# Performance work log

Measured on AMD Instinct MI355X. Metric: run time of the kernel, lower is better.

The kernel has to match this reference:

```python
import math
import jax, jax.numpy as jnp
import numpy as np

HEAD_DIM = 128
NUM_HEADS = 16
NUM_KV_HEADS = 4
CAUSAL = True


def rotate_half(x):
    x1 = x[..., : x.shape[-1] // 2]
    x2 = x[..., x.shape[-1] // 2 :]
    return jnp.concatenate([-x2, x1], axis=-1)


def setup_inputs() -> dict:
    key = jax.random.key(0)
    k1, k2, k3, k4, k5 = jax.random.split(key, 5)
    B, S, H = 2, 2048, 2048
    total_heads = NUM_HEADS + 2 * NUM_KV_HEADS  # 24
    hidden_states = jax.random.normal(k1, (B, S, H), dtype=jnp.float32)
    cos = jax.random.normal(k2, (S, HEAD_DIM), dtype=jnp.float32)
    sin = jax.random.normal(k3, (S, HEAD_DIM), dtype=jnp.float32)
    # eqx.nn.Linear weight layout: [out_features, in_features], y = W @ x
    w_qkv = jax.random.normal(k4, (total_heads * HEAD_DIM, H), dtype=jnp.float32) / math.sqrt(H)
    w_o = jax.random.normal(k5, (H, NUM_HEADS * HEAD_DIM), dtype=jnp.float32) / math.sqrt(NUM_HEADS * HEAD_DIM)
    return {"hidden_states": hidden_states, "cos": cos, "sin": sin, "w_qkv": w_qkv, "w_o": w_o}


def reference(hidden_states, cos, sin, w_qkv, w_o):
    B, S, _ = hidden_states.shape
    # fused QKV projection: [B,S,total_heads,head_dim]
    qkv = jnp.einsum("bsh,oh->bso", hidden_states, w_qkv).reshape(B, S, -1, HEAD_DIM)
    q = qkv[:, :, :NUM_HEADS]
    k = qkv[:, :, NUM_HEADS : NUM_HEADS + NUM_KV_HEADS]
    v = qkv[:, :, NUM_HEADS + NUM_KV_HEADS :]
    # RoPE: cos/sin [S,head_dim] -> broadcast [S,1,head_dim] over heads
    c = cos[..., None, :]
    s_ = sin[..., None, :]
    q = q * c + rotate_half(q) * s_
    k = k * c + rotate_half(k) * s_
    # GQA: repeat K/V across query-head groups
    rep = NUM_HEADS // NUM_KV_HEADS
    k = jnp.repeat(k, rep, axis=2)
    v = jnp.repeat(v, rep, axis=2)
    scale = 1.0 / math.sqrt(HEAD_DIM)
    scores = jnp.einsum("bshd,bthd->bhst", q, k) * scale  # [B,H,S,S]
    if CAUSAL:
        mask = jnp.tril(jnp.ones((S, S), dtype=bool))[None, None]
        scores = jnp.where(mask, scores, jnp.float32(-1e10))
    attn = jax.nn.softmax(scores, axis=-1)
    out = jnp.einsum("bhst,bthd->bshd", attn, v).reshape(B, S, -1)
    return jnp.einsum("bsd,od->bso", out, w_o)
```

## Files before the change

kernel.cpp:

```cpp
#include <hip/hip_runtime.h>
#include <hip/hip_bf16.h>
#include <stdint.h>

typedef __hip_bfloat16 bf16;
typedef __attribute__((ext_vector_type(8))) __bf16 bf16x8;
typedef __attribute__((ext_vector_type(4))) float f32x4;
typedef __attribute__((ext_vector_type(16))) float f32x16;
typedef __attribute__((ext_vector_type(4))) unsigned int u32x4;

#define QSCALE_LOG2E (0.08838834764831845f * 1.4426950408889634f)

__device__ __forceinline__ float fast_exp2(float x) {
#if __has_builtin(__builtin_amdgcn_exp2f)
  return __builtin_amdgcn_exp2f(x);
#else
  return exp2f(x);
#endif
}

__device__ __forceinline__ void gload_lds16(const void* g, void* l) {
  __builtin_amdgcn_global_load_lds(
      (__attribute__((address_space(1))) void*)(uintptr_t)g,
      (__attribute__((address_space(3))) void*)(uint32_t)(uintptr_t)l,
      16, 0, 0);
}

__global__ void cast3(const float* __restrict__ h, const float* __restrict__ wq,
                      const float* __restrict__ wo, bf16* __restrict__ oh,
                      bf16* __restrict__ owq, bf16* __restrict__ owo) {
  const int total = 4718592;
  const int stride = gridDim.x * blockDim.x;
  for (int c = blockIdx.x * blockDim.x + threadIdx.x; c < total; c += stride) {
    const float* src;
    bf16* dst;
    int i;
    if (c < 2097152) { src = h; dst = oh; i = c; }
    else if (c < 3670016) { src = wq; dst = owq; i = c - 2097152; }
    else { src = wo; dst = owo; i = c - 3670016; }
    float4 v = reinterpret_cast<const float4*>(src)[i];
    bf16 tmp[4];
    tmp[0] = __float2bfloat16(v.x);
    tmp[1] = __float2bfloat16(v.y);
    tmp[2] = __float2bfloat16(v.z);
    tmp[3] = __float2bfloat16(v.w);
    reinterpret_cast<uint2*>(dst)[i] = *reinterpret_cast<uint2*>(tmp);
  }
}

__device__ __forceinline__ void store_c(float v, bf16* p) { *p = __float2bfloat16(v); }
__device__ __forceinline__ void store_c(float v, float* p) { *p = v; }

__device__ __forceinline__ bf16x8 rd_swz(const bf16* base, int row, int ks, int hi) {
  const int byte = row * 128 + ((ks * 64 + hi * 16) ^ ((row & 7) << 4));
  return *reinterpret_cast<const bf16x8*>((const char*)base + byte);
}

__device__ __forceinline__ void stage_part(const bf16* __restrict__ g, int K,
                                           int kt, bf16* ldsBase, int part,
                                           int tid) {
  const int ga = part * 512 + tid;
  const int r = ga >> 3;
  const int gl = ga & 7;
  const int col = kt * 64 + ((gl ^ (r & 7)) << 3);
  gload_lds16(g + (size_t)r * K + col, (char*)ldsBase + ga * 16);
}

#define DS_A(QR)                                                              \
  _Pragma("unroll") for (int m = 0; m < 4; ++m)                               \
  _Pragma("unroll") for (int ks = 0; ks < 2; ++ks)                            \
      af[m][ks] = rd_swz(Acur, wm * 128 + (QR) * 64 + m * 16 + lr, ks, hi);

#define DS_B0()                                                               \
  _Pragma("unroll") for (int n = 0; n < NQ0; ++n)                             \
  _Pragma("unroll") for (int ks = 0; ks < 2; ++ks)                            \
      bf0[n][ks] = rd_swz(Bcur, wn * WN + n * 16 + lr, ks, hi);

#define DS_B1()                                                               \
  _Pragma("unroll") for (int n = 0; n < NQ1; ++n)                             \
  _Pragma("unroll") for (int ks = 0; ks < 2; ++ks)                            \
      bf1[n][ks] = rd_swz(Bcur, wn * WN + (NQ0 + n) * 16 + lr, ks, hi);

#define MFMA_Q0(QR)                                                           \
  __builtin_amdgcn_s_setprio(1);                                             \
  _Pragma("unroll") for (int ks = 0; ks < 2; ++ks)                            \
  _Pragma("unroll") for (int m = 0; m < 4; ++m)                               \
  _Pragma("unroll") for (int n = 0; n < NQ0; ++n)                             \
      acc[(QR) * 4 + m][n] = __builtin_amdgcn_mfma_f32_16x16x32_bf16(         \
          af[m][ks], bf0[n][ks], acc[(QR) * 4 + m][n], 0, 0, 0);              \
  __builtin_amdgcn_s_setprio(0);

#define MFMA_Q1(QR)                                                           \
  __builtin_amdgcn_s_setprio(1);                                             \
  _Pragma("unroll") for (int ks = 0; ks < 2; ++ks)                            \
  _Pragma("unroll") for (int m = 0; m < 4; ++m)                               \
  _Pragma("unroll") for (int n = 0; n < NQ1; ++n)                             \
      acc[(QR) * 4 + m][NQ0 + n] = __builtin_amdgcn_mfma_f32_16x16x32_bf16(   \
          af[m][ks], bf1[n][ks], acc[(QR) * 4 + m][NQ0 + n], 0, 0, 0);        \
  __builtin_amdgcn_s_setprio(0);

#define PHASE_SYNC_PRE()                                \
  __builtin_amdgcn_s_barrier();                         \
  asm volatile("s_waitcnt lgkmcnt(0)" ::: "memory");    \
  __builtin_amdgcn_sched_barrier(0);

#define PHASE_END() __builtin_amdgcn_s_barrier();

#define VMCNT_LB()                                                            \
  if constexpr (LB == 2) asm volatile("s_waitcnt vmcnt(2)" ::: "memory");     \
  else if constexpr (LB == 3) asm volatile("s_waitcnt vmcnt(3)" ::: "memory");\
  else asm volatile("s_waitcnt vmcnt(4)" ::: "memory");

template <int BN, typename OutT>
__global__ __launch_bounds__(512, 2) void gemm256(const bf16* __restrict__ A,
                                                  const bf16* __restrict__ B,
                                                  OutT* __restrict__ C,
                                                  int M, int N, int K, int NBX) {
  constexpr int NFRAG = BN / 64;
  constexpr int NQ0 = (NFRAG + 1) / 2;
  constexpr int NQ1 = NFRAG - NQ0;
  constexpr int WN = BN / 4;
  constexpr int LB = BN / 64;
  constexpr int LB0 = (LB + 1) / 2;
  constexpr int LB1 = LB - LB0;

  extern __shared__ bf16 sm[];
  bf16* A0 = sm;
  bf16* A1 = sm + 16384;
  bf16* B0 = sm + 32768;
  bf16* B1 = B0 + BN * 64;

  const int tid = threadIdx.x;
  const int lane = tid & 63;
  const int w = tid >> 6;
  const int wm = w >> 2;
  const int wn = w & 3;
  const int lr = lane & 15;
  const int hi = lane >> 4;

  const int nwg = gridDim.x;
  const int cpx = nwg >> 3;
  const int bid = blockIdx.x;
  const int wg = (bid & 7) * cpx + (bid >> 3);
  const int bx = wg % NBX;
  const int by = wg / NBX;
  const int row0 = by * 256;
  const int col0 = bx * BN;

  const bf16* Ag = A + (size_t)row0 * K;
  const bf16* Bg = B + (size_t)col0 * K;

#pragma unroll
  for (int p = 0; p < 4; ++p) stage_part(Ag, K, 0, A0, p, tid);
#pragma unroll
  for (int p = 0; p < LB; ++p) stage_part(Bg, K, 0, B0, p, tid);
#pragma unroll
  for (int p = 0; p < LB; ++p) stage_part(Bg, K, 1, B1, p, tid);
  VMCNT_LB();
  __builtin_amdgcn_s_barrier();

  f32x4 acc[8][NFRAG] = {};
  bf16x8 af[4][2], bf0[NQ0][2], bf1[NQ1 ? NQ1 : 1][2];

  const int iters = K >> 7;
  for (int i = 0; i < iters; ++i) {
    const bool g2 = (i + 1 < iters);
    const int t1 = 2 * i + 1, t2 = 2 * i + 2, t3 = 2 * i + 3;
    {
      const bf16* Acur = A0;
      const bf16* Bcur = B0;
      DS_A(0); DS_B0();
      stage_part(Ag, K, t1, A1, 0, tid);
      stage_part(Ag, K, t1, A1, 1, tid);
      PHASE_SYNC_PRE(); MFMA_Q0(0); PHASE_END();
      DS_B1();
      stage_part(Ag, K, t1, A1, 2, tid);
      stage_part(Ag, K, t1, A1, 3, tid);
      PHASE_SYNC_PRE(); MFMA_Q1(0); PHASE_END();
      DS_A(1);
      if (g2) {
#pragma unroll
        for (int p = 0; p < LB0; ++p) stage_part(Bg, K, t2, B0, p, tid);
      }
      PHASE_SYNC_PRE(); MFMA_Q0(1); PHASE_END();
      if (g2) {
#pragma unroll
        for (int p = 0; p < LB1; ++p) stage_part(Bg, K, t2, B0, LB0 + p, tid);
        VMCNT_LB();
      } else {
        asm volatile("s_waitcnt vmcnt(0)" ::: "memory");
      }
      PHASE_SYNC_PRE(); MFMA_Q1(1); PHASE_END();
    }
    {
      const bf16* Acur = A1;
      const bf16* Bcur = B1;
      DS_A(0); DS_B0();
      if (g2) {
        stage_part(Ag, K, t2, A0, 0, tid);
        stage_part(Ag, K, t2, A0, 1, tid);
      }
      PHASE_SYNC_PRE(); MFMA_Q0(0); PHASE_END();
      DS_B1();
      if (g2) {
        stage_part(Ag, K, t2, A0, 2, tid);
        stage_part(Ag, K, t2, A0, 3, tid);
      }
      PHASE_SYNC_PRE(); MFMA_Q1(0); PHASE_END();
      DS_A(1);
      if (g2) {
#pragma unroll
        for (int p = 0; p < LB0; ++p) stage_part(Bg, K, t3, B1, p, tid);
      }
      PHASE_SYNC_PRE(); MFMA_Q0(1); PHASE_END();
      if (g2) {
#pragma unroll
        for (int p = 0; p < LB1; ++p) stage_part(Bg, K, t3, B1, LB0 + p, tid);
        VMCNT_LB();
      } else {
        asm volatile("s_waitcnt vmcnt(0)" ::: "memory");
      }
      PHASE_SYNC_PRE(); MFMA_Q1(1); PHASE_END();
    }
  }

#pragma unroll
  for (int mi = 0; mi < 8; ++mi)
#pragma unroll
    for (int ni = 0; ni < NFRAG; ++ni)
#pragma unroll
      for (int j = 0; j < 4; ++j) {
        const int r = row0 + wm * 128 + mi * 16 + hi * 4 + j;
        const int cc = col0 + wn * WN + ni * 16 + lr;
        store_c(acc[mi][ni][j], &C[(size_t)r * N + cc]);
      }
}

__global__ __launch_bounds__(256) void rope_vtrans(const bf16* __restrict__ qkv,
                                                   const float* __restrict__ cs,
                                                   const float* __restrict__ sn,
                                                   bf16* __restrict__ Q,
                                                   bf16* __restrict__ Kd,
                                                   bf16* __restrict__ Vt) {
  __shared__ bf16 tile[64 * 136];
  const int bid = blockIdx.x;
  if (bid < 4096) {
    const int tok = bid;
    const int b = tok >> 11;
    const int s = tok & 2047;
    const bf16* row = qkv + (size_t)tok * 3072;
    for (int idx = threadIdx.x; idx < 1280; idx += blockDim.x) {
      const int head = idx >> 6;
      const int j = idx & 63;
      float x1 = __bfloat162float(row[head * 128 + j]);
      float x2 = __bfloat162float(row[head * 128 + j + 64]);
      const float c1 = cs[s * 128 + j];
      const float c2 = cs[s * 128 + j + 64];
      const float s1 = sn[s * 128 + j];
      const float s2 = sn[s * 128 + j + 64];
      float y1 = x1 * c1 - x2 * s1;
      float y2 = x2 * c2 + x1 * s2;
      bf16* dst;
      if (head < 16) {
        y1 *= QSCALE_LOG2E;
        y2 *= QSCALE_LOG2E;
        dst = Q + ((size_t)(b * 16 + head) * 2048 + s) * 128;
      } else {
        dst = Kd + ((size_t)(b * 4 + head - 16) * 2048 + s) * 128;
      }
      dst[j] = __float2bfloat16(y1);
      dst[j + 64] = __float2bfloat16(y2);
    }
  } else {
    const int vb = bid - 4096;
    const int stile = vb & 31;
    const int hv = (vb >> 5) & 3;
    const int b = vb >> 7;
    const int tid = threadIdx.x;
    const int tok0 = stile * 64;
    const bf16* src = qkv + (size_t)(b * 2048 + tok0) * 3072 + 2560 + hv * 128;
#pragma unroll
    for (int i = 0; i < 4; ++i) {
      const int c = tid + i * 256;
      const int r = c >> 4;
      const int off = (c & 15) * 8;
      uint4 d = *reinterpret_cast<const uint4*>(src + (size_t)r * 3072 + off);
      *reinterpret_cast<uint4*>(&tile[r * 136 + off]) = d;
    }
    __syncthreads();
    bf16* dst = Vt + ((size_t)(b * 4 + hv) * 128) * 2048 + tok0;
#pragma unroll
    for (int i = 0; i < 4; ++i) {
      const int o = tid + i * 256;
      const int d = o >> 3;
      const int s0 = (o & 7) * 8;
      bf16 vals[8];
#pragma unroll
      for (int j = 0; j < 8; ++j) vals[j] = tile[(s0 + j) * 136 + d];
      *reinterpret_cast<uint4*>(dst + (size_t)d * 2048 + s0) =
          *reinterpret_cast<const uint4*>(vals);
    }
  }
}

__device__ __forceinline__ void stage_k(const bf16* __restrict__ Kb, int k0,
                                        bf16* dst, int w, int lane) {
#pragma unroll
  for (int i = 0; i < 4; ++i) {
    const int L16 = i * 256 + w * 64 + lane;
    const int row = L16 >> 4;
    const int colb = (L16 & 15) * 16;
    const int src = colb ^ ((row & 7) << 4);
    gload_lds16(Kb + (size_t)(k0 + row) * 128 + (src >> 1),
                (char*)dst + (i * 256 + w * 64) * 16);
  }
}

__device__ __forceinline__ void stage_v(const bf16* __restrict__ Vtb, int k0,
                                        bf16* dst, int w, int lane) {
#pragma unroll
  for (int i = 0; i < 4; ++i) {
    const int L16 = i * 256 + w * 64 + lane;
    const int row = L16 >> 3;
    const int colb = (L16 & 7) * 16;
    const int src = colb ^ ((row & 7) << 4);
    gload_lds16(Vtb + (size_t)row * 2048 + k0 + (src >> 1),
                (char*)dst + (i * 256 + w * 64) * 16);
  }
}

__device__ __forceinline__ bf16x8 lds_read_swz(const bf16* base, int row,
                                               int colElem, int rowBytes) {
  const int byte = row * rowBytes + (((colElem * 2) ^ ((row & 7) << 4)));
  return *reinterpret_cast<const bf16x8*>((const char*)base + byte);
}

__global__ __launch_bounds__(256, 2) void attn_fwd(const bf16* __restrict__ Qg,
                                                   const bf16* __restrict__ Kg,
                                                   const bf16* __restrict__ Vtg,
                                                   bf16* __restrict__ Og) {
  __shared__ bf16 Ks[2][64 * 128];
  __shared__ bf16 Vs[2][128 * 64];

  const int tid = threadIdx.x;
  const int lane = tid & 63;
  const int w = tid >> 6;
  const int bid = blockIdx.x;
  int qt, bh;
  if (bid < 256) { qt = bid & 15; bh = bid >> 4; }
  else           { qt = 15 - (bid & 15); bh = 16 + ((bid - 256) >> 4); }
  const int b = bh >> 4;
  const int h = bh & 15;
  const int kvh = h >> 2;
  const int q31 = lane & 31;
  const int hw = lane >> 5;

  const bf16* Qb = Qg + ((size_t)(b * 16 + h) * 2048) * 128;
  const bf16* Kb = Kg + ((size_t)(b * 4 + kvh) * 2048) * 128;
  const bf16* Vtb = Vtg + ((size_t)(b * 4 + kvh) * 128) * 2048;

  const int qw = qt * 128 + w * 32;

  bf16x8 qf[8];
#pragma unroll
  for (int db = 0; db < 8; ++db)
    qf[db] = *reinterpret_cast<const bf16x8*>(Qb + (size_t)(qw + q31) * 128 +
                                              db * 16 + hw * 8);

  f32x16 acc[4] = {};
  float mrow = -1e30f;
  float lsum = 0.f;

  const int nt = 2 * qt + 2;

  stage_k(Kb, 0, &Ks[0][0], w, lane);
  stage_v(Vtb, 0, &Vs[0][0], w, lane);

  for (int t = 0; t < nt; ++t) {
    const int cur = t & 1;
    if (t + 1 < nt) {
      stage_k(Kb, (t + 1) * 64, &Ks[cur ^ 1][0], w, lane);
      stage_v(Vtb, (t + 1) * 64, &Vs[cur ^ 1][0], w, lane);
      asm volatile("s_waitcnt vmcnt(8)" ::: "memory");
    } else {
      asm volatile("s_waitcnt vmcnt(0)" ::: "memory");
    }
    __builtin_amdgcn_s_barrier();
    __builtin_amdgcn_sched_barrier(0);

    const int k0 = t * 64;
    const bool active = (k0 <= qw + 31);
    if (active) {
      const bf16* Kt = &Ks[cur][0];
      const bf16* Vtl = &Vs[cur][0];

      f32x16 sacc[2] = {};
#pragma unroll
      for (int kb = 0; kb < 2; ++kb)
#pragma unroll
        for (int db = 0; db < 8; ++db) {
          bf16x8 kf = lds_read_swz(Kt, kb * 32 + q31, db * 16 + hw * 8, 256);
          sacc[kb] = __builtin_amdgcn_mfma_f32_32x32x16_bf16(kf, qf[db],
                                                             sacc[kb], 0, 0, 0);
        }

      float p[2][16];
#pragma unroll
      for (int kb = 0; kb < 2; ++kb)
#pragma unroll
        for (int r = 0; r < 16; ++r) p[kb][r] = sacc[kb][r];

      if (k0 + 63 > qw) {
        const int qg = qw + q31;
#pragma unroll
        for (int kb = 0; kb < 2; ++kb)
#pragma unroll
          for (int r = 0; r < 16; ++r) {
            const int k = k0 + kb * 32 + (r & 3) + 8 * (r >> 2) + 4 * hw;
            if (k > qg) p[kb][r] = -1e30f;
          }
      }

      float mt = p[0][0];
#pragma unroll
      for (int r = 1; r < 16; ++r) mt = fmaxf(mt, p[0][r]);
#pragma unroll
      for (int r = 0; r < 16; ++r) mt = fmaxf(mt, p[1][r]);
      mt = fmaxf(mt, __shfl_xor(mt, 32));

      if (__any(mt > mrow + 11.5f)) {
        const float mnew = fmaxf(mrow, mt);
        const float alpha = fast_exp2(mrow - mnew);
        mrow = mnew;
        lsum *= alpha;
        float areg[16];
#pragma unroll
        for (int r = 0; r < 16; ++r) {
          const int qloc = (r & 3) + 8 * (r >> 2) + 4 * hw;
          areg[r] = __shfl(alpha, qloc + (lane & 32));
        }
#pragma unroll
        for (int db = 0; db < 4; ++db)
#pragma unroll
          for (int r = 0; r < 16; ++r) acc[db][r] *= areg[r];
      }

      float rs = 0.f;
#pragma unroll
      for (int kb = 0; kb < 2; ++kb)
#pragma unroll
        for (int r = 0; r < 16; ++r) {
          const float pe = fast_exp2(p[kb][r] - mrow);
          p[kb][r] = pe;
          rs += pe;
        }
      rs += __shfl_xor(rs, 32);
      lsum += rs;

      unsigned int pk[2][8];
#pragma unroll
      for (int kb = 0; kb < 2; ++kb)
#pragma unroll
        for (int i = 0; i < 8; ++i)
          asm("v_cvt_pk_bf16_f32 %0, %1, %2"
              : "=v"(pk[kb][i])
              : "v"(p[kb][2 * i]), "v"(p[kb][2 * i + 1]));

#pragma unroll
      for (int kb16 = 0; kb16 < 4; ++kb16) {
        const int kb = kb16 >> 1;
        const int j0 = (kb16 & 1) * 4;
        unsigned int a0 = pk[kb][j0 + 0], b0 = pk[kb][j0 + 2];
        unsigned int a1 = pk[kb][j0 + 1], b1 = pk[kb][j0 + 3];
        asm volatile("v_permlane32_swap_b32 %0, %1" : "+v"(a0), "+v"(b0));
        asm volatile("v_permlane32_swap_b32 %0, %1" : "+v"(a1), "+v"(b1));
        u32x4 afu;
        afu.x = a0; afu.y = a1; afu.z = b0; afu.w = b1;
        bf16x8 pa;
        __builtin_memcpy(&pa, &afu, 16);
#pragma unroll
        for (int db = 0; db < 4; ++db) {
          bf16x8 vf = lds_read_swz(Vtl, db * 32 + q31, kb16 * 16 + hw * 8, 128);
          acc[db] = __builtin_amdgcn_mfma_f32_32x32x16_bf16(pa, vf,
                                                            acc[db], 0, 0, 0);
        }
      }
    }

    __builtin_amdgcn_sched_barrier(0);
    __builtin_amdgcn_s_barrier();
  }

  const float inv = 1.0f / lsum;
  float invq[16];
#pragma unroll
  for (int r = 0; r < 16; ++r) {
    const int qloc = (r & 3) + 8 * (r >> 2) + 4 * hw;
    invq[r] = __shfl(inv, qloc + (lane & 32));
  }
#pragma unroll
  for (int db = 0; db < 4; ++db)
#pragma unroll
    for (int r = 0; r < 16; ++r) {
      const int qg = qw + (r & 3) + 8 * (r >> 2) + 4 * hw;
      const int dg = db * 32 + q31;
      Og[((size_t)(b * 2048 + qg)) * 2048 + h * 128 + dg] =
          __float2bfloat16(acc[db][r] * invq[r]);
    }
}

extern "C" void kernel_launch(void* const* d_in, const int* in_sizes, int n_in,
                              void* d_out, int out_size, void* d_ws,
                              size_t ws_size, hipStream_t stream) {
  const float* hidden = (const float*)d_in[0];
  const float* cs = (const float*)d_in[1];
  const float* sn = (const float*)d_in[2];
  const float* wqkv = (const float*)d_in[3];
  const float* wo = (const float*)d_in[4];
  float* out = (float*)d_out;

  bf16* p = (bf16*)d_ws;
  bf16* hid_b = p;   p += 8388608;
  bf16* wqkv_b = p;  p += 6291456;
  bf16* wo_b = p;    p += 4194304;
  bf16* qkv = p;     p += 12582912;
  bf16* Qs = p;      p += 8388608;
  bf16* Ksc = p;     p += 2097152;
  bf16* Vt = p;      p += 2097152;

  (void)hipFuncSetAttribute((const void*)gemm256<192, bf16>,
                            hipFuncAttributeMaxDynamicSharedMemorySize, 131072);
  (void)hipFuncSetAttribute((const void*)gemm256<128, float>,
                            hipFuncAttributeMaxDynamicSharedMemorySize, 131072);

  cast3<<<2048, 256, 0, stream>>>(hidden, wqkv, wo, hid_b, wqkv_b, wo_b);

  gemm256<192, bf16><<<256, 512, 114688, stream>>>(hid_b, wqkv_b, qkv,
                                                   4096, 3072, 2048, 16);
  rope_vtrans<<<4352, 256, 0, stream>>>(qkv, cs, sn, Qs, Ksc, Vt);

  bf16* aout = hid_b;
  attn_fwd<<<512, 256, 0, stream>>>(Qs, Ksc, Vt, aout);

  gemm256<128, float><<<256, 512, 98304, stream>>>(aout, wo_b, out,
                                                   4096, 2048, 2048, 16);
}
```

Measured before the change: 173.1 us.

## Store transposed V in 8-token chunked layout for contiguous LDS staging

The V transpose kernel now writes V in a blocked layout: for each group of 8 tokens, every head-dim row holds a contiguous 16-byte chunk. The attention kernel stages V tiles with fully contiguous 16-byte global-to-LDS loads and reads LDS fragments without the XOR swizzle. This is meant to improve global coalescing for V loads, since the old layout used strided 2048-element rows, and to drop the swizzle arithmetic. LDS reads are now unswizzled, which could raise bank conflicts.

Result: no change. 171.5 us (-0.9%).

```diff
diff --git a/kernel.cpp b/kernel.cpp
--- a/kernel.cpp
+++ b/kernel.cpp
@@ -287,16 +287,17 @@
       *reinterpret_cast<uint4*>(&tile[r * 136 + off]) = d;
     }
     __syncthreads();
-    bf16* dst = Vt + ((size_t)(b * 4 + hv) * 128) * 2048 + tok0;
+    bf16* dst8 = Vt + ((size_t)(b * 4 + hv) * 128) * 2048;
 #pragma unroll
     for (int i = 0; i < 4; ++i) {
       const int o = tid + i * 256;
-      const int d = o >> 3;
-      const int s0 = (o & 7) * 8;
+      const int kgl = o >> 7;
+      const int d = o & 127;
       bf16 vals[8];
 #pragma unroll
-      for (int j = 0; j < 8; ++j) vals[j] = tile[(s0 + j) * 136 + d];
-      *reinterpret_cast<uint4*>(dst + (size_t)d * 2048 + s0) =
+      for (int j = 0; j < 8; ++j) vals[j] = tile[(kgl * 8 + j) * 136 + d];
+      const size_t chunk = ((size_t)(tok0 >> 3) + kgl) * 128 + d;
+      *reinterpret_cast<uint4*>(dst8 + chunk * 8) =
           *reinterpret_cast<const uint4*>(vals);
     }
   }
@@ -315,16 +316,15 @@
   }
 }
 
-__device__ __forceinline__ void stage_v(const bf16* __restrict__ Vtb, int k0,
+__device__ __forceinline__ void stage_v(const bf16* __restrict__ Vt8b, int k0,
                                         bf16* dst, int w, int lane) {
 #pragma unroll
   for (int i = 0; i < 4; ++i) {
-    const int L16 = i * 256 + w * 64 + lane;
-    const int row = L16 >> 3;
-    const int colb = (L16 & 7) * 16;
-    const int src = colb ^ ((row & 7) << 4);
-    gload_lds16(Vtb + (size_t)row * 2048 + k0 + (src >> 1),
-                (char*)dst + (i * 256 + w * 64) * 16);
+    const int ga = i * 256 + w * 64 + lane;
+    const int kgl = ga >> 7;
+    const int d = ga & 127;
+    const size_t chunk = ((size_t)(k0 >> 3) + kgl) * 128 + d;
+    gload_lds16(Vt8b + chunk * 8, (char*)dst + ga * 16);
   }
 }
 
@@ -356,7 +356,7 @@
 
   const bf16* Qb = Qg + ((size_t)(b * 16 + h) * 2048) * 128;
   const bf16* Kb = Kg + ((size_t)(b * 4 + kvh) * 2048) * 128;
-  const bf16* Vtb = Vtg + ((size_t)(b * 4 + kvh) * 128) * 2048;
+  const bf16* Vt8b = Vtg + ((size_t)(b * 4 + kvh) * 128) * 2048;
 
   const int qw = qt * 128 + w * 32;
 
@@ -373,13 +373,13 @@
   const int nt = 2 * qt + 2;
 
   stage_k(Kb, 0, &Ks[0][0], w, lane);
-  stage_v(Vtb, 0, &Vs[0][0], w, lane);
+  stage_v(Vt8b, 0, &Vs[0][0], w, lane);
 
   for (int t = 0; t < nt; ++t) {
     const int cur = t & 1;
     if (t + 1 < nt) {
       stage_k(Kb, (t + 1) * 64, &Ks[cur ^ 1][0], w, lane);
-      stage_v(Vtb, (t + 1) * 64, &Vs[cur ^ 1][0], w, lane);
+      stage_v(Vt8b, (t + 1) * 64, &Vs[cur ^ 1][0], w, lane);
       asm volatile("s_waitcnt vmcnt(8)" ::: "memory");
     } else {
       asm volatile("s_waitcnt vmcnt(0)" ::: "memory");
@@ -479,7 +479,10 @@
         __builtin_memcpy(&pa, &afu, 16);
 #pragma unroll
         for (int db = 0; db < 4; ++db) {
-          bf16x8 vf = lds_read_swz(Vtl, db * 32 + q31, kb16 * 16 + hw * 8, 128);
+          const int kgl = kb16 * 2 + hw;
+          const int d = db * 32 + q31;
+          bf16x8 vf = *reinterpret_cast<const bf16x8*>(
+              (const char*)Vtl + (kgl * 128 + d) * 16);
           acc[db] = __builtin_amdgcn_mfma_f32_32x32x16_bf16(pa, vf,
                                                             acc[db], 0, 0, 0);
         }
```
